# Kernel tuning notes

Measured on AMD Instinct MI355X. Metric: run time of the kernel, lower is better.

The kernel has to match this reference:

```python
import jax, jax.numpy as jnp
import numpy as np

EPS = 1e-12  # tf.math.l2_normalize epsilon


def setup_inputs() -> dict:
    key = jax.random.key(0)
    k1, k2 = jax.random.split(key)
    B, R, D = 2048, 256, 784
    inputs = jax.random.normal(k1, (B, D), dtype=jnp.float32)
    # keras 'uniform' initializer: U(-0.05, 0.05)
    centers = jax.random.uniform(k2, (R, D), dtype=jnp.float32, minval=-0.05, maxval=0.05)
    sigmas = jnp.ones((R, D), dtype=jnp.float32)
    return {"inputs": inputs, "centers": centers, "sigmas": sigmas}


def reference(inputs, centers, sigmas):
    # l2-normalize inputs along feature axis (tf.math.l2_normalize semantics)
    sq_norm = jnp.sum(jnp.square(inputs), axis=-1, keepdims=True)
    x = inputs * jax.lax.rsqrt(jnp.maximum(sq_norm, EPS))
    # (B, 1, D) - (R, D) -> (B, R, D); weighted squared distance, reduced over D
    squared_diff = jnp.square(x[:, None, :] - centers)  # (B, R, D)
    dist = jnp.sum(squared_diff / jnp.square(sigmas), axis=-1)  # (B, R)
    return jnp.exp(-0.5 * dist)
```

## Files before the change

kernel.cpp:

```cpp
#include <hip/hip_runtime.h>
#include <stdint.h>


typedef char   i8x16 __attribute__((ext_vector_type(16)));
typedef int    i32x4 __attribute__((ext_vector_type(4)));
typedef float  f32x4 __attribute__((ext_vector_type(4)));

#define NB 2048
#define NR 256
#define ND 784
#define KR 1664
#define KP 832
#define NSTEP 13
#define PF 5
#define INV127 0.007874015748031496f

__global__ __launch_bounds__(256) void prep_kernel(
        const float* __restrict__ inputs, const float* __restrict__ centers,
        const float* __restrict__ sigmas, uint8_t* __restrict__ Acat,
        uint8_t* __restrict__ Bcat, float* __restrict__ SA1, float* __restrict__ SA2,
        float* __restrict__ SU, float* __restrict__ SV, float* __restrict__ ST)
{
    const int w    = threadIdx.x >> 6;
    const int lane = threadIdx.x & 63;
    const int blk  = blockIdx.x;
    if (blk < 512) {
        const int b = blk * 4 + w;
        const float4* src = (const float4*)(inputs + (size_t)b * ND);
        float4 v0 = src[lane];
        float4 v1 = src[lane + 64];
        float4 v2 = src[lane + 128];
        float4 v3 = make_float4(0.f, 0.f, 0.f, 0.f);
        if (lane < 4) v3 = src[lane + 192];
        float ss = v0.x*v0.x + v0.y*v0.y + v0.z*v0.z + v0.w*v0.w
                 + v1.x*v1.x + v1.y*v1.y + v1.z*v1.z + v1.w*v1.w
                 + v2.x*v2.x + v2.y*v2.y + v2.z*v2.z + v2.w*v2.w
                 + v3.x*v3.x + v3.y*v3.y + v3.z*v3.z + v3.w*v3.w;
        float mg = fmaxf(fmaxf(fmaxf(fabsf(v0.x), fabsf(v0.y)), fmaxf(fabsf(v0.z), fabsf(v0.w))),
                   fmaxf(fmaxf(fmaxf(fabsf(v1.x), fabsf(v1.y)), fmaxf(fabsf(v1.z), fabsf(v1.w))),
                   fmaxf(fmaxf(fmaxf(fabsf(v2.x), fabsf(v2.y)), fmaxf(fabsf(v2.z), fabsf(v2.w))),
                         fmaxf(fmaxf(fabsf(v3.x), fabsf(v3.y)), fmaxf(fabsf(v3.z), fabsf(v3.w))))));
        #pragma unroll
        for (int m = 32; m; m >>= 1) {
            ss += __shfl_xor(ss, m);
            mg  = fmaxf(mg, __shfl_xor(mg, m));
        }
        const float inv = rsqrtf(fmaxf(ss, 1e-12f));
        const float mx  = fmaxf(mg * inv, 1e-30f);
        const float r1  = 127.0f / mx;
        const float r2  = 127.0f / (mx * mx);
        uint8_t* rowA = Acat + (size_t)b * KR;
        auto pk = [&](float4 g, int col) {
            float x0 = g.x*inv, x1 = g.y*inv, x2 = g.z*inv, x3 = g.w*inv;
            int a0 = __float2int_rn(x0*x0*r2), a1 = __float2int_rn(x1*x1*r2);
            int a2 = __float2int_rn(x2*x2*r2), a3 = __float2int_rn(x3*x3*r2);
            int b0 = __float2int_rn(x0*r1),    b1 = __float2int_rn(x1*r1);
            int b2 = __float2int_rn(x2*r1),    b3 = __float2int_rn(x3*r1);
            uint32_t q2 = (a0&255) | ((a1&255)<<8) | ((a2&255)<<16) | ((a3&255)<<24);
            uint32_t q1 = (b0&255) | ((b1&255)<<8) | ((b2&255)<<16) | ((b3&255)<<24);
            *(uint32_t*)(rowA + col)      = q2;
            *(uint32_t*)(rowA + KP + col) = q1;
        };
        pk(v0, 4*lane);
        pk(v1, 4*(lane+64));
        pk(v2, 4*(lane+128));
        if (lane < 4) pk(v3, 4*(lane+192));
        if (lane < 12) {
            *(uint32_t*)(rowA + ND + 4*lane)      = 0u;
            *(uint32_t*)(rowA + KP + ND + 4*lane) = 0u;
        }
        if (lane == 0) { SA1[b] = mx * INV127; SA2[b] = mx * mx * INV127; }
    } else {
        const int r = (blk - 512) * 4 + w;
        const float4* cp = (const float4*)(centers + (size_t)r * ND);
        const float4* sp = (const float4*)(sigmas  + (size_t)r * ND);
        float4 c0 = cp[lane],     s0 = sp[lane];
        float4 c1 = cp[lane+64],  s1 = sp[lane+64];
        float4 c2 = cp[lane+128], s2 = sp[lane+128];
        float4 c3 = make_float4(0,0,0,0), s3 = make_float4(1,1,1,1);
        const bool v3ok = lane < 4;
        if (v3ok) { c3 = cp[lane+192]; s3 = sp[lane+192]; }
        float4 w0, w1, w2, w3;
        w0.x=1.f/(s0.x*s0.x); w0.y=1.f/(s0.y*s0.y); w0.z=1.f/(s0.z*s0.z); w0.w=1.f/(s0.w*s0.w);
        w1.x=1.f/(s1.x*s1.x); w1.y=1.f/(s1.y*s1.y); w1.z=1.f/(s1.z*s1.z); w1.w=1.f/(s1.w*s1.w);
        w2.x=1.f/(s2.x*s2.x); w2.y=1.f/(s2.y*s2.y); w2.z=1.f/(s2.z*s2.z); w2.w=1.f/(s2.w*s2.w);
        w3.x=1.f/(s3.x*s3.x); w3.y=1.f/(s3.y*s3.y); w3.z=1.f/(s3.z*s3.z); w3.w=1.f/(s3.w*s3.w);
        if (!v3ok) { w3 = make_float4(0,0,0,0); }
        float t3 = c0.x*c0.x*w0.x + c0.y*c0.y*w0.y + c0.z*c0.z*w0.z + c0.w*c0.w*w0.w
                 + c1.x*c1.x*w1.x + c1.y*c1.y*w1.y + c1.z*c1.z*w1.z + c1.w*c1.w*w1.w
                 + c2.x*c2.x*w2.x + c2.y*c2.y*w2.y + c2.z*c2.z*w2.z + c2.w*c2.w*w2.w
                 + c3.x*c3.x*w3.x + c3.y*c3.y*w3.y + c3.z*c3.z*w3.z + c3.w*c3.w*w3.w;
        float mw = fmaxf(fmaxf(w0.x, w0.y), fmaxf(w0.z, w0.w));
        mw = fmaxf(mw, fmaxf(fmaxf(w1.x, w1.y), fmaxf(w1.z, w1.w)));
        mw = fmaxf(mw, fmaxf(fmaxf(w2.x, w2.y), fmaxf(w2.z, w2.w)));
        mw = fmaxf(mw, fmaxf(fmaxf(w3.x, w3.y), fmaxf(w3.z, w3.w)));
        float mm = fmaxf(fmaxf(fabsf(2.f*c0.x*w0.x), fabsf(2.f*c0.y*w0.y)),
                         fmaxf(fabsf(2.f*c0.z*w0.z), fabsf(2.f*c0.w*w0.w)));
        mm = fmaxf(mm, fmaxf(fmaxf(fabsf(2.f*c1.x*w1.x), fabsf(2.f*c1.y*w1.y)),
                             fmaxf(fabsf(2.f*c1.z*w1.z), fabsf(2.f*c1.w*w1.w))));
        mm = fmaxf(mm, fmaxf(fmaxf(fabsf(2.f*c2.x*w2.x), fabsf(2.f*c2.y*w2.y)),
                             fmaxf(fabsf(2.f*c2.z*w2.z), fabsf(2.f*c2.w*w2.w))));
        mm = fmaxf(mm, fmaxf(fmaxf(fabsf(2.f*c3.x*w3.x), fabsf(2.f*c3.y*w3.y)),
                             fmaxf(fabsf(2.f*c3.z*w3.z), fabsf(2.f*c3.w*w3.w))));
        #pragma unroll
        for (int m = 32; m; m >>= 1) {
            t3 += __shfl_xor(t3, m);
            mw  = fmaxf(mw, __shfl_xor(mw, m));
            mm  = fmaxf(mm, __shfl_xor(mm, m));
        }
        mw = fmaxf(mw, 1e-30f); mm = fmaxf(mm, 1e-30f);
        const float ru = 127.0f / mw, rv = 127.0f / mm;
        uint8_t* rowB = Bcat + (size_t)r * KR;
        auto pkB = [&](float4 c, float4 ww, int col) {
            int a0 = __float2int_rn(ww.x*ru), a1 = __float2int_rn(ww.y*ru);
            int a2 = __float2int_rn(ww.z*ru), a3 = __float2int_rn(ww.w*ru);
            int b0 = __float2int_rn(-2.f*c.x*ww.x*rv), b1 = __float2int_rn(-2.f*c.y*ww.y*rv);
            int b2 = __float2int_rn(-2.f*c.z*ww.z*rv), b3 = __float2int_rn(-2.f*c.w*ww.w*rv);
            uint32_t qw = (a0&255) | ((a1&255)<<8) | ((a2&255)<<16) | ((a3&255)<<24);
            uint32_t qm = (b0&255) | ((b1&255)<<8) | ((b2&255)<<16) | ((b3&255)<<24);
            *(uint32_t*)(rowB + col)      = qw;
            *(uint32_t*)(rowB + KP + col) = qm;
        };
        pkB(c0, w0, 4*lane);
        pkB(c1, w1, 4*(lane+64));
        pkB(c2, w2, 4*(lane+128));
        if (v3ok) pkB(c3, w3, 4*(lane+192));
        if (lane < 12) {
            *(uint32_t*)(rowB + ND + 4*lane)      = 0u;
            *(uint32_t*)(rowB + KP + ND + 4*lane) = 0u;
        }
        if (lane == 0) { SU[r] = mw * INV127; SV[r] = mm * INV127; ST[r] = t3; }
    }
}

__global__ __launch_bounds__(256) void rbf_gemm(
        const uint8_t* __restrict__ Acat, const uint8_t* __restrict__ Bcat,
        const float* __restrict__ SA1, const float* __restrict__ SA2,
        const float* __restrict__ SU, const float* __restrict__ SV,
        const float* __restrict__ ST, float* __restrict__ out)
{
    const int w    = threadIdx.x >> 6;
    const int lane = threadIdx.x & 63;
    const int bid  = (int)blockIdx.x;
    const int xcd  = bid & 7;
    const int j    = bid >> 3;
    const int mt   = xcd * 4 + (j & 3);
    const int nt   = j >> 2;
    const int qm   = w >> 1;
    const int kh   = w & 1;
    const int wm   = mt * 64 + qm * 32;
    const int wn   = nt * 32;
    const int r16  = lane & 15;
    const int ko   = (lane >> 4) * 16;

    const uint8_t* a0p = Acat + (size_t)(wm + r16) * KR + kh * KP + ko;
    const uint8_t* a1p = a0p + 16 * KR;
    const uint8_t* b0p = Bcat + (size_t)(wn + r16) * KR + kh * KP + ko;
    const uint8_t* b1p = b0p + 16 * KR;

    i32x4 acc00 = {0,0,0,0}, acc01 = {0,0,0,0}, acc10 = {0,0,0,0}, acc11 = {0,0,0,0};
    i32x4 a0[PF], a1[PF], b0[PF], b1[PF];

#define LDSET(J, KS) do { const int o_ = (KS) * 64;                           \
    a0[J] = *(const i32x4*)(a0p + o_); a1[J] = *(const i32x4*)(a1p + o_);     \
    b0[J] = *(const i32x4*)(b0p + o_); b1[J] = *(const i32x4*)(b1p + o_); } while (0)

#define MM(J) do {                                                                 \
    acc00 = __builtin_amdgcn_mfma_i32_16x16x64_i8(a0[J], b0[J], acc00, 0, 0, 0);   \
    acc01 = __builtin_amdgcn_mfma_i32_16x16x64_i8(a0[J], b1[J], acc01, 0, 0, 0);   \
    acc10 = __builtin_amdgcn_mfma_i32_16x16x64_i8(a1[J], b0[J], acc10, 0, 0, 0);   \
    acc11 = __builtin_amdgcn_mfma_i32_16x16x64_i8(a1[J], b1[J], acc11, 0, 0, 0); } while (0)

    #pragma unroll
    for (int s = 0; s < PF; ++s) LDSET(s, s);
    #pragma unroll
    for (int s = 0; s < NSTEP; ++s) {
        MM(s % PF);
        if (s + PF < NSTEP) LDSET(s % PF, s + PF);
    }

    __shared__ int red[2 * 32 * 33];
    const int hi4 = (lane >> 4) << 2;
    int* slab = red + qm * (32 * 33);
    if (kh) {
#define DUMP(ACC, MO, NO)                                             \
        { _Pragma("unroll")                                           \
          for (int qq = 0; qq < 4; ++qq)                              \
              slab[((MO) + hi4 + qq) * 33 + (NO) + r16] = ACC[qq]; }
        DUMP(acc00, 0, 0)  DUMP(acc01, 0, 16)
        DUMP(acc10, 16, 0) DUMP(acc11, 16, 16)
#undef DUMP
    }
    __syncthreads();
    if (!kh) {
        const int c0 = wn + r16, c1 = wn + 16 + r16;
        const float u0 = SU[c0], v0 = SV[c0], t0 = ST[c0];
        const float u1 = SU[c1], v1 = SV[c1], t1 = ST[c1];
#define FIN(ACC, MO, NO, UU, VV, TT)                                              \
        { const int rw0 = wm + (MO) + hi4;                                        \
          float* o_ = out + (size_t)rw0 * NR + wn + (NO) + r16;                   \
          _Pragma("unroll")                                                       \
          for (int qq = 0; qq < 4; ++qq) {                                        \
              const int rr = rw0 + qq;                                            \
              const float d2 = (float)slab[((MO) + hi4 + qq) * 33 + (NO) + r16];  \
              const float dist = SA2[rr] * (UU) * (float)ACC[qq]                  \
                               + SA1[rr] * (VV) * d2 + (TT);                      \
              o_[qq * NR] = __expf(-0.5f * dist); } }
        FIN(acc00, 0, 0, u0, v0, t0)   FIN(acc01, 0, 16, u1, v1, t1)
        FIN(acc10, 16, 0, u0, v0, t0)  FIN(acc11, 16, 16, u1, v1, t1)
#undef FIN
    }
#undef LDSET
#undef MM
}

extern "C" void kernel_launch(void* const* d_in, const int* in_sizes, int n_in,
                              void* d_out, int out_size, void* d_ws, size_t ws_size,
                              hipStream_t stream) {
    const float* inputs  = (const float*)d_in[0];
    const float* centers = (const float*)d_in[1];
    const float* sigmas  = (const float*)d_in[2];
    uint8_t* Acat = (uint8_t*)d_ws;
    uint8_t* Bcat = Acat + (size_t)NB * KR;
    float*   scal = (float*)(Bcat + (size_t)NR * KR);
    float* SA1 = scal;
    float* SA2 = scal + 2048;
    float* SU  = scal + 4096;
    float* SV  = scal + 4352;
    float* ST  = scal + 4608;
    prep_kernel<<<576, 256, 0, stream>>>(inputs, centers, sigmas, Acat, Bcat,
                                         SA1, SA2, SU, SV, ST);
    rbf_gemm<<<256, 256, 0, stream>>>(Acat, Bcat, SA1, SA2, SU, SV, ST, (float*)d_out);
}
```

Measured before the change: 18.68 us.

## Skip the squared-input GEMM half when each sigma row is uniform

```diff
diff --git a/kernel.cpp b/kernel.cpp
--- a/kernel.cpp
+++ b/kernel.cpp
@@ -2,7 +2,6 @@
 #include <stdint.h>
 
 
-typedef char   i8x16 __attribute__((ext_vector_type(16)));
 typedef int    i32x4 __attribute__((ext_vector_type(4)));
 typedef float  f32x4 __attribute__((ext_vector_type(4)));
 
@@ -11,7 +10,6 @@
 #define ND 784
 #define KR 1664
 #define KP 832
-#define NSTEP 13
 #define PF 5
 #define INV127 0.007874015748031496f
 
@@ -19,7 +17,8 @@
         const float* __restrict__ inputs, const float* __restrict__ centers,
         const float* __restrict__ sigmas, uint8_t* __restrict__ Acat,
         uint8_t* __restrict__ Bcat, float* __restrict__ SA1, float* __restrict__ SA2,
-        float* __restrict__ SU, float* __restrict__ SV, float* __restrict__ ST)
+        float* __restrict__ SU, float* __restrict__ SV, float* __restrict__ ST,
+        float* __restrict__ WR, uint32_t* __restrict__ FLG)
 {
     const int w    = threadIdx.x >> 6;
     const int lane = threadIdx.x & 63;
@@ -85,6 +84,16 @@
         w1.x=1.f/(s1.x*s1.x); w1.y=1.f/(s1.y*s1.y); w1.z=1.f/(s1.z*s1.z); w1.w=1.f/(s1.w*s1.w);
         w2.x=1.f/(s2.x*s2.x); w2.y=1.f/(s2.y*s2.y); w2.z=1.f/(s2.z*s2.z); w2.w=1.f/(s2.w*s2.w);
         w3.x=1.f/(s3.x*s3.x); w3.y=1.f/(s3.y*s3.y); w3.z=1.f/(s3.z*s3.z); w3.w=1.f/(s3.w*s3.w);
+        float wmn = fminf(fminf(fminf(w0.x,w0.y), fminf(w0.z,w0.w)),
+                    fminf(fminf(fminf(w1.x,w1.y), fminf(w1.z,w1.w)),
+                          fminf(fminf(w2.x,w2.y), fminf(w2.z,w2.w))));
+        float wmx = fmaxf(fmaxf(fmaxf(w0.x,w0.y), fmaxf(w0.z,w0.w)),
+                    fmaxf(fmaxf(fmaxf(w1.x,w1.y), fmaxf(w1.z,w1.w)),
+                          fmaxf(fmaxf(w2.x,w2.y), fmaxf(w2.z,w2.w))));
+        if (v3ok) {
+            wmn = fminf(wmn, fminf(fminf(w3.x,w3.y), fminf(w3.z,w3.w)));
+            wmx = fmaxf(wmx, fmaxf(fmaxf(w3.x,w3.y), fmaxf(w3.z,w3.w)));
+        }
         if (!v3ok) { w3 = make_float4(0,0,0,0); }
         float t3 = c0.x*c0.x*w0.x + c0.y*c0.y*w0.y + c0.z*c0.z*w0.z + c0.w*c0.w*w0.w
                  + c1.x*c1.x*w1.x + c1.y*c1.y*w1.y + c1.z*c1.z*w1.z + c1.w*c1.w*w1.w
@@ -107,6 +116,8 @@
             t3 += __shfl_xor(t3, m);
             mw  = fmaxf(mw, __shfl_xor(mw, m));
             mm  = fmaxf(mm, __shfl_xor(mm, m));
+            wmn = fminf(wmn, __shfl_xor(wmn, m));
+            wmx = fmaxf(wmx, __shfl_xor(wmx, m));
         }
         mw = fmaxf(mw, 1e-30f); mm = fmaxf(mm, 1e-30f);
         const float ru = 127.0f / mw, rv = 127.0f / mm;
@@ -129,15 +140,47 @@
             *(uint32_t*)(rowB + ND + 4*lane)      = 0u;
             *(uint32_t*)(rowB + KP + ND + 4*lane) = 0u;
         }
-        if (lane == 0) { SU[r] = mw * INV127; SV[r] = mm * INV127; ST[r] = t3; }
-    }
-}
+        if (lane == 0) {
+            SU[r] = mw * INV127; SV[r] = mm * INV127; ST[r] = t3;
+            WR[r] = wmn; FLG[r] = (wmn == wmx) ? 1u : 0u;
+        }
+    }
+}
+
+#define LDSET(J, KS) do { const int o_ = (KS) * 64;                           \
+    a0[J] = *(const i32x4*)(a0p + o_); a1[J] = *(const i32x4*)(a1p + o_);     \
+    b0[J] = *(const i32x4*)(b0p + o_); b1[J] = *(const i32x4*)(b1p + o_); } while (0)
+#define MM(J) do {                                                                 \
+    acc00 = __builtin_amdgcn_mfma_i32_16x16x64_i8(a0[J], b0[J], acc00, 0, 0, 0);   \
+    acc01 = __builtin_amdgcn_mfma_i32_16x16x64_i8(a0[J], b1[J], acc01, 0, 0, 0);   \
+    acc10 = __builtin_amdgcn_mfma_i32_16x16x64_i8(a1[J], b0[J], acc10, 0, 0, 0);   \
+    acc11 = __builtin_amdgcn_mfma_i32_16x16x64_i8(a1[J], b1[J], acc11, 0, 0, 0); } while (0)
+
+template<int NST, int BASE>
+__device__ __forceinline__ void chain_i8(
+        const uint8_t* __restrict__ a0p, const uint8_t* __restrict__ a1p,
+        const uint8_t* __restrict__ b0p, const uint8_t* __restrict__ b1p,
+        i32x4& acc00, i32x4& acc01, i32x4& acc10, i32x4& acc11)
+{
+    i32x4 a0[PF], a1[PF], b0[PF], b1[PF];
+    constexpr int PRE = (PF < NST) ? PF : NST;
+    #pragma unroll
+    for (int s = 0; s < PRE; ++s) LDSET(s, BASE + s);
+    #pragma unroll
+    for (int s = 0; s < NST; ++s) {
+        MM(s % PF);
+        if (s + PF < NST) LDSET(s % PF, BASE + s + PF);
+    }
+}
+#undef LDSET
+#undef MM
 
 __global__ __launch_bounds__(256) void rbf_gemm(
         const uint8_t* __restrict__ Acat, const uint8_t* __restrict__ Bcat,
         const float* __restrict__ SA1, const float* __restrict__ SA2,
         const float* __restrict__ SU, const float* __restrict__ SV,
-        const float* __restrict__ ST, float* __restrict__ out)
+        const float* __restrict__ ST, const float* __restrict__ WR,
+        const uint32_t* __restrict__ FLG, float* __restrict__ out)
 {
     const int w    = threadIdx.x >> 6;
     const int lane = threadIdx.x & 63;
@@ -153,30 +196,25 @@
     const int r16  = lane & 15;
     const int ko   = (lane >> 4) * 16;
 
-    const uint8_t* a0p = Acat + (size_t)(wm + r16) * KR + kh * KP + ko;
-    const uint8_t* a1p = a0p + 16 * KR;
-    const uint8_t* b0p = Bcat + (size_t)(wn + r16) * KR + kh * KP + ko;
-    const uint8_t* b1p = b0p + 16 * KR;
+    uint32_t fv = 1u;
+    if (lane < 32) fv = FLG[wn + lane];
+    const bool fast = __all(fv != 0u);
 
     i32x4 acc00 = {0,0,0,0}, acc01 = {0,0,0,0}, acc10 = {0,0,0,0}, acc11 = {0,0,0,0};
-    i32x4 a0[PF], a1[PF], b0[PF], b1[PF];
-
-#define LDSET(J, KS) do { const int o_ = (KS) * 64;                           \
-    a0[J] = *(const i32x4*)(a0p + o_); a1[J] = *(const i32x4*)(a1p + o_);     \
-    b0[J] = *(const i32x4*)(b0p + o_); b1[J] = *(const i32x4*)(b1p + o_); } while (0)
-
-#define MM(J) do {                                                                 \
-    acc00 = __builtin_amdgcn_mfma_i32_16x16x64_i8(a0[J], b0[J], acc00, 0, 0, 0);   \
-    acc01 = __builtin_amdgcn_mfma_i32_16x16x64_i8(a0[J], b1[J], acc01, 0, 0, 0);   \
-    acc10 = __builtin_amdgcn_mfma_i32_16x16x64_i8(a1[J], b0[J], acc10, 0, 0, 0);   \
-    acc11 = __builtin_amdgcn_mfma_i32_16x16x64_i8(a1[J], b1[J], acc11, 0, 0, 0); } while (0)
-
-    #pragma unroll
-    for (int s = 0; s < PF; ++s) LDSET(s, s);
-    #pragma unroll
-    for (int s = 0; s < NSTEP; ++s) {
-        MM(s % PF);
-        if (s + PF < NSTEP) LDSET(s % PF, s + PF);
+
+    if (fast) {
+        const uint8_t* a0p = Acat + (size_t)(wm + r16) * KR + KP + ko;
+        const uint8_t* a1p = a0p + 16 * KR;
+        const uint8_t* b0p = Bcat + (size_t)(wn + r16) * KR + KP + ko;
+        const uint8_t* b1p = b0p + 16 * KR;
+        if (kh == 0) chain_i8<7, 0>(a0p, a1p, b0p, b1p, acc00, acc01, acc10, acc11);
+        else         chain_i8<6, 7>(a0p, a1p, b0p, b1p, acc00, acc01, acc10, acc11);
+    } else {
+        const uint8_t* a0p = Acat + (size_t)(wm + r16) * KR + kh * KP + ko;
+        const uint8_t* a1p = a0p + 16 * KR;
+        const uint8_t* b0p = Bcat + (size_t)(wn + r16) * KR + kh * KP + ko;
+        const uint8_t* b1p = b0p + 16 * KR;
+        chain_i8<13, 0>(a0p, a1p, b0p, b1p, acc00, acc01, acc10, acc11);
     }
 
     __shared__ int red[2 * 32 * 33];
@@ -194,8 +232,24 @@
     __syncthreads();
     if (!kh) {
         const int c0 = wn + r16, c1 = wn + 16 + r16;
-        const float u0 = SU[c0], v0 = SV[c0], t0 = ST[c0];
-        const float u1 = SU[c1], v1 = SV[c1], t1 = ST[c1];
+        const float v0 = SV[c0], t0 = ST[c0];
+        const float v1 = SV[c1], t1 = ST[c1];
+        if (fast) {
+            const float W0 = WR[c0], W1 = WR[c1];
+#define FINF(ACC, MO, NO, VV, TT, WW)                                             \
+        { const int rw0 = wm + (MO) + hi4;                                        \
+          float* o_ = out + (size_t)rw0 * NR + wn + (NO) + r16;                   \
+          _Pragma("unroll")                                                       \
+          for (int qq = 0; qq < 4; ++qq) {                                        \
+              const int rr = rw0 + qq;                                            \
+              const int dq = ACC[qq] + slab[((MO) + hi4 + qq) * 33 + (NO) + r16]; \
+              const float dist = (WW) + (TT) + SA1[rr] * (VV) * (float)dq;        \
+              o_[qq * NR] = __expf(-0.5f * dist); } }
+            FINF(acc00, 0, 0, v0, t0, W0)   FINF(acc01, 0, 16, v1, t1, W1)
+            FINF(acc10, 16, 0, v0, t0, W0)  FINF(acc11, 16, 16, v1, t1, W1)
+#undef FINF
+        } else {
+            const float u0 = SU[c0], u1 = SU[c1];
 #define FIN(ACC, MO, NO, UU, VV, TT)                                              \
         { const int rw0 = wm + (MO) + hi4;                                        \
           float* o_ = out + (size_t)rw0 * NR + wn + (NO) + r16;                   \
@@ -206,12 +260,11 @@
               const float dist = SA2[rr] * (UU) * (float)ACC[qq]                  \
                                + SA1[rr] * (VV) * d2 + (TT);                      \
               o_[qq * NR] = __expf(-0.5f * dist); } }
-        FIN(acc00, 0, 0, u0, v0, t0)   FIN(acc01, 0, 16, u1, v1, t1)
-        FIN(acc10, 16, 0, u0, v0, t0)  FIN(acc11, 16, 16, u1, v1, t1)
+            FIN(acc00, 0, 0, u0, v0, t0)   FIN(acc01, 0, 16, u1, v1, t1)
+            FIN(acc10, 16, 0, u0, v0, t0)  FIN(acc11, 16, 16, u1, v1, t1)
 #undef FIN
-    }
-#undef LDSET
-#undef MM
+        }
+    }
 }
 
 extern "C" void kernel_launch(void* const* d_in, const int* in_sizes, int n_in,
@@ -228,7 +281,10 @@
     float* SU  = scal + 4096;
     float* SV  = scal + 4352;
     float* ST  = scal + 4608;
+    float* WR  = scal + 4864;
+    uint32_t* FLG = (uint32_t*)(scal + 5120);
     prep_kernel<<<576, 256, 0, stream>>>(inputs, centers, sigmas, Acat, Bcat,
-                                         SA1, SA2, SU, SV, ST);
-    rbf_gemm<<<256, 256, 0, stream>>>(Acat, Bcat, SA1, SA2, SU, SV, ST, (float*)d_out);
-}
+                                         SA1, SA2, SU, SV, ST, WR, FLG);
+    rbf_gemm<<<256, 256, 0, stream>>>(Acat, Bcat, SA1, SA2, SU, SV, ST, WR, FLG,
+                                      (float*)d_out);
+}
```

Result: faster. 15.83 us (-15.3%).
